# Kernel tuning notes

Hardware: AMD Instinct MI355X
Metric: run time of the kernel (lower is better)

Reference implementation:

```python
import math
import jax, jax.numpy as jnp
import numpy as np

NH = 16          # num attention heads
NOPE = 128       # qk_nope_head_dim
ROPE = 64        # qk_rope_head_dim
VD = 128         # v_head_dim
QLR = 1536       # q_lora_rank
IH = 8           # index_n_heads
ID = 128         # index_head_dim
TOPK = 8         # index_topk
EPS = 1e-5


def layernorm(x, w, b):
    mu = jnp.mean(x, axis=-1, keepdims=True)
    var = jnp.mean((x - mu) ** 2, axis=-1, keepdims=True)
    return (x - mu) * jax.lax.rsqrt(var + EPS) * w + b


def rope_tables(dim, end, base=10000.0):
    freqs = 1.0 / (base ** (jnp.arange(0, dim, 2, dtype=jnp.float32) / dim))  # [dim//2]
    t = jnp.arange(end, dtype=jnp.float32)
    f = jnp.outer(t, freqs)  # [end, dim//2]
    return jnp.cos(f), jnp.sin(f)


def apply_rope(x, cos, sin):
    # x: [b, h, s, d]; cos/sin: [s, d//2] (interleaved real/imag pairs)
    xr, xi = x[..., 0::2], x[..., 1::2]
    c = cos[None, None, :, :]
    s = sin[None, None, :, :]
    or_, oi = xr * c - xi * s, xr * s + xi * c
    return jnp.stack([or_, oi], axis=-1).reshape(x.shape)


def setup_inputs() -> dict:
    key = jax.random.key(0)
    ks = jax.random.split(key, 16)
    H = 2048
    B, S = 2, 2048
    w = lambda k, shp: (jax.random.normal(k, shp, dtype=jnp.float32) * 0.02)
    return {
        "x": jax.random.normal(ks[0], (B, S, H), dtype=jnp.float32),
        "W_cq": w(ks[1], (H, QLR)),
        "q_norm_w": jnp.ones((QLR,), jnp.float32),
        "q_norm_b": jnp.zeros((QLR,), jnp.float32),
        "W_q": w(ks[2], (QLR, NH * (NOPE + ROPE))),
        "W_ckv": w(ks[3], (H, NH * (NOPE + ROPE))),
        "kv_norm_w": jnp.ones((NOPE,), jnp.float32),
        "kv_norm_b": jnp.zeros((NOPE,), jnp.float32),
        "W_kv": w(ks[4], (NOPE, NOPE + VD)),
        "W_o": w(ks[5], (NH * VD, H)),
        "W_ip": w(ks[6], (H, IH * ID)),
        "W_ig": w(ks[7], (H, IH)),
        "W_sq": w(ks[8], (ID, ID)),
        "W_sk": w(ks[9], (ID, ID)),
        "W_sv": w(ks[10], (ID, ID)),
        "W_io": w(ks[11], (ID, H)),
    }


def _forward(x, W_cq, q_norm_w, q_norm_b, W_q, W_ckv, kv_norm_w, kv_norm_b,
             W_kv, W_o, W_ip, W_ig, W_sq, W_sk, W_sv, W_io):
    B, S, H = x.shape
    # --- MLA dense path ---
    qc = layernorm(x @ W_cq, q_norm_w, q_norm_b)                  # [B,S,QLR]
    qp = (qc @ W_q).reshape(B, S, NH, NOPE + ROPE).transpose(0, 2, 1, 3)
    q_nope, q_pe = qp[..., :NOPE], qp[..., NOPE:]
    kvc = (x @ W_ckv).reshape(B, S, NH, ROPE + NOPE).transpose(0, 2, 1, 3)
    k_pe, kv_nope = kvc[..., :ROPE], kvc[..., ROPE:]
    kv_n = layernorm(kv_nope, kv_norm_w, kv_norm_b)               # [B,NH,S,NOPE]
    kvp = kv_n @ W_kv                                             # [B,NH,S,NOPE+VD]
    k_nope, v = kvp[..., :NOPE], kvp[..., NOPE:]
    cos, sin = rope_tables(ROPE, S)
    q_pe = apply_rope(q_pe, cos, sin)
    k_pe = apply_rope(k_pe, cos, sin)
    q = jnp.concatenate([q_nope, q_pe], axis=-1)                  # [B,NH,S,192]
    k = jnp.concatenate([k_nope, k_pe], axis=-1)
    scale = 1.0 / math.sqrt(NOPE + ROPE)
    scores = jnp.einsum("bhqd,bhkd->bhqk", q, k) * scale
    causal = jnp.triu(jnp.ones((S, S), dtype=bool), k=1)
    scores = jnp.where(causal[None, None], -jnp.inf, scores)
    probs = jax.nn.softmax(scores.astype(jnp.float32), axis=-1).astype(q.dtype)
    attn = jnp.einsum("bhqk,bhkd->bhqd", probs, v)                # [B,NH,S,VD]
    # --- NSA sparse path (lightning indexer) ---
    ist = (x @ W_ip).reshape(B, S, IH, ID).transpose(0, 2, 1, 3)  # [B,IH,S,ID]
    gate = (x @ W_ig).transpose(0, 2, 1)                          # [B,IH,S]
    _, top_idx = jax.lax.top_k(gate, TOPK)                        # [B,IH,TOPK]
    sel = jnp.take_along_axis(ist, top_idx[..., None], axis=2)    # [B,IH,TOPK,ID]
    sq, sk, sv = sel @ W_sq, sel @ W_sk, sel @ W_sv
    ss = jnp.einsum("bhqd,bhkd->bhqk", sq, sk) / math.sqrt(ID)    # [B,IH,TOPK,TOPK]
    sp = jax.nn.softmax(ss.astype(jnp.float32), axis=-1).astype(sq.dtype)
    so = jnp.einsum("bhqk,bhkd->bhqd", sp, sv)                    # [B,IH,TOPK,ID]
    sparse_out = so @ W_io                                        # [B,IH,TOPK,H]
    io = sparse_out.mean(axis=2)[:, :, None, :VD]                 # [B,IH,1,VD]
    io = jnp.broadcast_to(io, (B, IH, S, VD))
    io = jnp.repeat(io, NH // IH, axis=1)                         # [B,NH,S,VD]
    attn = attn + io
    out = attn.transpose(0, 2, 1, 3).reshape(B, S, NH * VD) @ W_o
    return out


def reference(x, W_cq, q_norm_w, q_norm_b, W_q, W_ckv, kv_norm_w, kv_norm_b,
              W_kv, W_o, W_ip, W_ig, W_sq, W_sk, W_sv, W_io):
    return _forward(x, W_cq, q_norm_w, q_norm_b, W_q, W_ckv, kv_norm_w,
                    kv_norm_b, W_kv, W_o, W_ip, W_ig, W_sq, W_sk, W_sv, W_io)
```

## Files before the change

kernel.cpp:

```cpp
#include <hip/hip_runtime.h>
#include <hip/hip_bf16.h>
#include <math.h>

#define NH    16
#define NOPE  128
#define ROPED 64
#define VD    128
#define QLR   1536
#define IH    8
#define ID    128
#define TOPK  8
#define EPSF  1e-5f
#define B_    2
#define S_    2048
#define H_    2048

using bf16 = __hip_bfloat16;
typedef __attribute__((ext_vector_type(8))) short short8;
typedef __attribute__((ext_vector_type(4))) short short4v;
typedef __attribute__((ext_vector_type(4))) float f32x4;

#define GLOBAL_AS __attribute__((address_space(1)))
#define LDS_AS    __attribute__((address_space(3)))

__device__ __forceinline__ float b2f(bf16 v) { return __bfloat162float(v); }
__device__ __forceinline__ bf16 f2b(float v) { return __float2bfloat16(v); }
__device__ __forceinline__ void stoC(float* p, float v) { *p = v; }
__device__ __forceinline__ void stoC(bf16* p, float v) { *p = __float2bfloat16(v); }

__global__ __launch_bounds__(256) void gate_k(const float* __restrict__ x,
                                              const float* __restrict__ Wg,
                                              float* __restrict__ gate) {
    const int t = threadIdx.x;
    const int wid = t >> 6, lane = t & 63;
    const int row = blockIdx.x * 4 + wid;
    const float* xp = x + (size_t)row * H_;

    float acc[8] = {};
    for (int k0 = 0; k0 < H_; k0 += 256) {
        const int kb = k0 + lane * 4;
        const f32x4 xv = *(const f32x4*)(xp + kb);
        const f32x4 w0 = *(const f32x4*)(Wg + (size_t)kb * 8);
        const f32x4 w1 = *(const f32x4*)(Wg + (size_t)kb * 8 + 4);
        const f32x4 w2 = *(const f32x4*)(Wg + (size_t)(kb + 1) * 8);
        const f32x4 w3 = *(const f32x4*)(Wg + (size_t)(kb + 1) * 8 + 4);
        const f32x4 w4 = *(const f32x4*)(Wg + (size_t)(kb + 2) * 8);
        const f32x4 w5 = *(const f32x4*)(Wg + (size_t)(kb + 2) * 8 + 4);
        const f32x4 w6 = *(const f32x4*)(Wg + (size_t)(kb + 3) * 8);
        const f32x4 w7 = *(const f32x4*)(Wg + (size_t)(kb + 3) * 8 + 4);
#pragma unroll
        for (int j = 0; j < 4; j++) {
            acc[j]     += xv[0] * w0[j] + xv[1] * w2[j] + xv[2] * w4[j] + xv[3] * w6[j];
            acc[4 + j] += xv[0] * w1[j] + xv[1] * w3[j] + xv[2] * w5[j] + xv[3] * w7[j];
        }
    }
#pragma unroll
    for (int j = 0; j < 8; j++) {
#pragma unroll
        for (int off = 32; off > 0; off >>= 1)
            acc[j] += __shfl_xor(acc[j], off);
    }
    if (lane == 0) {
#pragma unroll
        for (int j = 0; j < 8; j++) gate[(size_t)row * 8 + j] = acc[j];
    }
}

template <typename OT>
__global__ __launch_bounds__(256) void gemm_bt_mfma_k(const bf16* __restrict__ A,
                                                      const bf16* __restrict__ Bt,
                                                      OT* __restrict__ C,
                                                      int M, int N, int K) {
    __shared__ bf16 As[128 * 32];
    __shared__ bf16 Bs[128 * 32];
    const int t = threadIdx.x;
    const int w = t >> 6;
    const int l = t & 63;
    const int col = l & 15;
    const int quad = l >> 4;
    const int wm = w >> 1, wn = w & 1;

    const int gx = gridDim.x;
    const int nwg = gx * gridDim.y;
    const int lin = blockIdx.y * gx + blockIdx.x;
    const int work = (lin & 7) * (nwg >> 3) + (lin >> 3);
    const int row0 = (work / gx) * 128;
    const int col0 = (work % gx) * 128;

    const int rA = l >> 2;
    const int cA = (l & 3) * 8;
    const bf16* ga0 = A + (size_t)(row0 + w * 16 + rA) * K + cA;
    const bf16* ga1 = A + (size_t)(row0 + (4 + w) * 16 + rA) * K + cA;
    const bf16* gb0 = Bt + (size_t)(col0 + w * 16 + rA) * K + cA;
    const bf16* gb1 = Bt + (size_t)(col0 + (4 + w) * 16 + rA) * K + cA;
    bf16* lA0 = &As[w * 512];
    bf16* lA1 = &As[(4 + w) * 512];
    bf16* lB0 = &Bs[w * 512];
    bf16* lB1 = &Bs[(4 + w) * 512];

    f32x4 acc[4][4];
#pragma unroll
    for (int i = 0; i < 4; i++)
#pragma unroll
        for (int j = 0; j < 4; j++) acc[i][j] = (f32x4){0.f, 0.f, 0.f, 0.f};

    for (int k0 = 0; k0 < K; k0 += 32) {
        __syncthreads();
        __builtin_amdgcn_global_load_lds((const GLOBAL_AS void*)(ga0 + k0),
                                         (LDS_AS void*)lA0, 16, 0, 0);
        __builtin_amdgcn_global_load_lds((const GLOBAL_AS void*)(ga1 + k0),
                                         (LDS_AS void*)lA1, 16, 0, 0);
        __builtin_amdgcn_global_load_lds((const GLOBAL_AS void*)(gb0 + k0),
                                         (LDS_AS void*)lB0, 16, 0, 0);
        __builtin_amdgcn_global_load_lds((const GLOBAL_AS void*)(gb1 + k0),
                                         (LDS_AS void*)lB1, 16, 0, 0);
        __syncthreads();

        short8 af[4], bfr[4];
#pragma unroll
        for (int i = 0; i < 4; i++) {
            af[i]  = *(const short8*)&As[(wm * 64 + i * 16 + col) * 32 + quad * 8];
            bfr[i] = *(const short8*)&Bs[(wn * 64 + i * 16 + col) * 32 + quad * 8];
        }
#pragma unroll
        for (int i = 0; i < 4; i++)
#pragma unroll
            for (int j = 0; j < 4; j++)
                acc[i][j] = __builtin_amdgcn_mfma_f32_16x16x32_bf16(af[i], bfr[j], acc[i][j], 0, 0, 0);
    }

#pragma unroll
    for (int i = 0; i < 4; i++)
#pragma unroll
        for (int j = 0; j < 4; j++)
#pragma unroll
            for (int r = 0; r < 4; r++) {
                const int gr = row0 + wm * 64 + i * 16 + quad * 4 + r;
                const int gc = col0 + wn * 64 + j * 16 + col;
                stoC(C + (size_t)gr * N + gc, acc[i][j][r]);
            }
}

__global__ __launch_bounds__(256) void gemm_kv_k(const bf16* __restrict__ A,
                                                 const bf16* __restrict__ Bt,
                                                 bf16* __restrict__ kvc,
                                                 bf16* __restrict__ VbT) {
    __shared__ bf16 As[128 * 32];
    __shared__ bf16 Bs[128 * 32];
    const int K = 128;
    const int t = threadIdx.x;
    const int w = t >> 6;
    const int l = t & 63;
    const int col = l & 15;
    const int quad = l >> 4;
    const int wm = w >> 1, wn = w & 1;

    const int gx = gridDim.x;
    const int nwg = gx * gridDim.y;
    const int lin = blockIdx.y * gx + blockIdx.x;
    const int work = (lin & 7) * (nwg >> 3) + (lin >> 3);
    const int row0 = (work / gx) * 128;
    const int col0 = (work % gx) * 128;

    const int rA = l >> 2;
    const int cA = (l & 3) * 8;
    const bf16* ga0 = A + (size_t)(row0 + w * 16 + rA) * K + cA;
    const bf16* ga1 = A + (size_t)(row0 + (4 + w) * 16 + rA) * K + cA;
    const bf16* gb0 = Bt + (size_t)(col0 + w * 16 + rA) * K + cA;
    const bf16* gb1 = Bt + (size_t)(col0 + (4 + w) * 16 + rA) * K + cA;
    bf16* lA0 = &As[w * 512];
    bf16* lA1 = &As[(4 + w) * 512];
    bf16* lB0 = &Bs[w * 512];
    bf16* lB1 = &Bs[(4 + w) * 512];

    f32x4 acc[4][4];
#pragma unroll
    for (int i = 0; i < 4; i++)
#pragma unroll
        for (int j = 0; j < 4; j++) acc[i][j] = (f32x4){0.f, 0.f, 0.f, 0.f};

    for (int k0 = 0; k0 < K; k0 += 32) {
        __syncthreads();
        __builtin_amdgcn_global_load_lds((const GLOBAL_AS void*)(ga0 + k0),
                                         (LDS_AS void*)lA0, 16, 0, 0);
        __builtin_amdgcn_global_load_lds((const GLOBAL_AS void*)(ga1 + k0),
                                         (LDS_AS void*)lA1, 16, 0, 0);
        __builtin_amdgcn_global_load_lds((const GLOBAL_AS void*)(gb0 + k0),
                                         (LDS_AS void*)lB0, 16, 0, 0);
        __builtin_amdgcn_global_load_lds((const GLOBAL_AS void*)(gb1 + k0),
                                         (LDS_AS void*)lB1, 16, 0, 0);
        __syncthreads();

        short8 af[4], bfr[4];
#pragma unroll
        for (int i = 0; i < 4; i++) {
            af[i]  = *(const short8*)&As[(wm * 64 + i * 16 + col) * 32 + quad * 8];
            bfr[i] = *(const short8*)&Bs[(wn * 64 + i * 16 + col) * 32 + quad * 8];
        }
#pragma unroll
        for (int i = 0; i < 4; i++)
#pragma unroll
            for (int j = 0; j < 4; j++)
                acc[i][j] = __builtin_amdgcn_mfma_f32_16x16x32_bf16(af[i], bfr[j], acc[i][j], 0, 0, 0);
    }

    if (col0 == 0) {
#pragma unroll
        for (int i = 0; i < 4; i++)
#pragma unroll
            for (int j = 0; j < 4; j++)
#pragma unroll
                for (int r = 0; r < 4; r++) {
                    const int gr = row0 + wm * 64 + i * 16 + quad * 4 + r;
                    const int gc = wn * 64 + j * 16 + col;
                    kvc[(size_t)gr * 192 + gc] = f2b(acc[i][j][r]);
                }
    } else {
        const int bb = row0 >> 15;
        const int ssb = ((row0 >> 4) & (S_ - 1)) + wm * 4;
#pragma unroll
        for (int j = 0; j < 4; j++) {
            const int dv = wn * 64 + j * 16 + col;
#pragma unroll
            for (int r = 0; r < 4; r++) {
                const int hh = quad * 4 + r;
                short4v pk;
#pragma unroll
                for (int i = 0; i < 4; i++) {
                    bf16 v = f2b(acc[i][j][r]);
                    pk[i] = *(short*)&v;
                }
                *(short4v*)&VbT[((size_t)(bb * NH + hh) * 128 + dv) * S_ + ssb] = pk;
            }
        }
    }
}

__global__ __launch_bounds__(256) void kv_ln_k(bf16* __restrict__ kvc,
                                               const float* __restrict__ knw,
                                               const float* __restrict__ knb,
                                               bf16* __restrict__ kvn) {
    const int idx = blockIdx.x * 4 + (threadIdx.x >> 6);
    const int lane = threadIdx.x & 63;
    const int s = (idx >> 4) & (S_ - 1);
    const size_t base = (size_t)idx * 192;

    const float v0 = b2f(kvc[base + 64 + lane]);
    const float v1 = b2f(kvc[base + 128 + lane]);
    float xr = 0.f, xi = 0.f;
    if (lane < 32) { xr = b2f(kvc[base + 2 * lane]); xi = b2f(kvc[base + 2 * lane + 1]); }

    float s1 = v0 + v1, s2 = v0 * v0 + v1 * v1;
#pragma unroll
    for (int off = 32; off > 0; off >>= 1) {
        s1 += __shfl_xor(s1, off);
        s2 += __shfl_xor(s2, off);
    }
    const float mu = s1 * (1.f / 128.f);
    const float rinv = rsqrtf(s2 * (1.f / 128.f) - mu * mu + EPSF);
    kvn[(size_t)idx * 128 + lane]      = f2b((v0 - mu) * rinv * knw[lane] + knb[lane]);
    kvn[(size_t)idx * 128 + lane + 64] = f2b((v1 - mu) * rinv * knw[lane + 64] + knb[lane + 64]);

    if (lane < 32) {
        const float freq = exp2f(-0.41524101186092014f * (float)lane);
        const float ang = (float)s * freq;
        float sn, c; sincosf(ang, &sn, &c);
        kvc[base + 128 + 2 * lane]     = f2b(xr * c - xi * sn);
        kvc[base + 128 + 2 * lane + 1] = f2b(xr * sn + xi * c);
    }
}

__global__ __launch_bounds__(256) void cast_bf16_k(const float* __restrict__ X,
                                                   bf16* __restrict__ Y, int n4) {
    for (int i = blockIdx.x * 256 + threadIdx.x; i < n4; i += gridDim.x * 256) {
        const f32x4 v = ((const f32x4*)X)[i];
        short4v o;
#pragma unroll
        for (int j = 0; j < 4; j++) {
            bf16 b = f2b(v[j]);
            o[j] = *(short*)&b;
        }
        ((short4v*)Y)[i] = o;
    }
}

__global__ __launch_bounds__(256) void transpose_cast_k(const float* __restrict__ W,
                                                        bf16* __restrict__ Wt,
                                                        int K, int N) {
    __shared__ float tile[32][33];
    const int t = threadIdx.x;
    const int tx = t & 31, ty = t >> 5;
    const int n0 = blockIdx.x * 32;
    const int k0 = blockIdx.y * 32;
#pragma unroll
    for (int i = 0; i < 4; i++)
        tile[ty + 8 * i][tx] = W[(size_t)(k0 + ty + 8 * i) * N + n0 + tx];
    __syncthreads();
#pragma unroll
    for (int i = 0; i < 4; i++)
        Wt[(size_t)(n0 + ty + 8 * i) * K + k0 + tx] = f2b(tile[tx][ty + 8 * i]);
}

__global__ __launch_bounds__(256) void layernorm_cast_k(const float* __restrict__ X,
                                                        const float* __restrict__ w,
                                                        const float* __restrict__ b,
                                                        bf16* __restrict__ Y,
                                                        int L) {
    __shared__ float r1[256], r2[256];
    const int row = blockIdx.x;
    const int t = threadIdx.x;
    const float* xp = X + (size_t)row * L;
    bf16* yp = Y + (size_t)row * L;
    float s1 = 0.f, s2 = 0.f;
    for (int j = t; j < L; j += 256) { const float v = xp[j]; s1 += v; s2 += v * v; }
    r1[t] = s1; r2[t] = s2; __syncthreads();
    for (int off = 128; off > 0; off >>= 1) {
        if (t < off) { r1[t] += r1[t + off]; r2[t] += r2[t + off]; }
        __syncthreads();
    }
    const float mu   = r1[0] / (float)L;
    const float var  = r2[0] / (float)L - mu * mu;
    const float rinv = rsqrtf(var + EPSF);
    for (int j = t; j < L; j += 256)
        yp[j] = f2b((xp[j] - mu) * rinv * w[j] + b[j]);
}

__global__ __launch_bounds__(256) void q_rope_k(bf16* __restrict__ qp) {
    const int total = B_ * S_ * NH * 32;
    for (int p = blockIdx.x * 256 + threadIdx.x; p < total; p += gridDim.x * 256) {
        const int j = p & 31;
        const int row = p >> 5;
        const int sr = row >> 4;
        const int s = sr & (S_ - 1);
        const size_t base = (size_t)row * 192 + 128 + 2 * j;
        const float xr = b2f(qp[base]);
        const float xi = b2f(qp[base + 1]);
        const float freq = exp2f(-0.41524101186092014f * (float)j);
        const float ang = (float)s * freq;
        float sn, c; sincosf(ang, &sn, &c);
        qp[base]     = f2b(xr * c - xi * sn);
        qp[base + 1] = f2b(xr * sn + xi * c);
    }
}

__global__ __launch_bounds__(256) void sparse_k(const float* __restrict__ gate,
                                                const float* __restrict__ ist,
                                                const float* __restrict__ Wsq,
                                                const float* __restrict__ Wsk,
                                                const float* __restrict__ Wsv,
                                                const float* __restrict__ Wio,
                                                float* __restrict__ io) {
    __shared__ float g[S_];
    __shared__ float sel[TOPK][ID];
    __shared__ float sq[TOPK][ID], sk[TOPK][ID], sv[TOPK][ID];
    __shared__ float sp[TOPK][TOPK];
    __shared__ float ms[ID];
    __shared__ float rv[256];
    __shared__ int ri[256];
    __shared__ int sidx[TOPK];
    const int bi = blockIdx.x;
    const int ih = bi % IH;
    const int b = bi / IH;
    const int t = threadIdx.x;

    for (int s = t; s < S_; s += 256) g[s] = gate[(size_t)(b * S_ + s) * IH + ih];
    __syncthreads();

    for (int r = 0; r < TOPK; r++) {
        float bv = -INFINITY; int bx = S_;
        for (int s = t; s < S_; s += 256) {
            const float v = g[s];
            if (v > bv) { bv = v; bx = s; }
        }
        rv[t] = bv; ri[t] = bx; __syncthreads();
        for (int off = 128; off > 0; off >>= 1) {
            if (t < off) {
                const float v2 = rv[t + off]; const int i2 = ri[t + off];
                if (v2 > rv[t] || (v2 == rv[t] && i2 < ri[t])) { rv[t] = v2; ri[t] = i2; }
            }
            __syncthreads();
        }
        if (t == 0) { sidx[r] = ri[0]; g[ri[0]] = -INFINITY; }
        __syncthreads();
    }

    for (int i = t; i < TOPK * ID; i += 256) {
        const int r = i >> 7, d = i & 127;
        sel[r][d] = ist[((size_t)(b * S_ + sidx[r]) * IH + ih) * ID + d];
    }
    __syncthreads();

    for (int i = t; i < TOPK * ID; i += 256) {
        const int r = i >> 7, n = i & 127;
        float aq = 0.f, ak = 0.f, av = 0.f;
        for (int k = 0; k < 128; k++) {
            const float s = sel[r][k];
            aq += s * Wsq[k * ID + n];
            ak += s * Wsk[k * ID + n];
            av += s * Wsv[k * ID + n];
        }
        sq[r][n] = aq; sk[r][n] = ak; sv[r][n] = av;
    }
    __syncthreads();

    if (t < TOPK * TOPK) {
        const int r = t >> 3, c = t & 7;
        float a = 0.f;
        for (int k = 0; k < 128; k++) a += sq[r][k] * sk[c][k];
        sp[r][c] = a * 0.08838834764831845f;
    }
    __syncthreads();

    if (t < TOPK) {
        float m = -INFINITY;
        for (int c = 0; c < 8; c++) m = fmaxf(m, sp[t][c]);
        float e[8]; float sum = 0.f;
        for (int c = 0; c < 8; c++) { e[c] = expf(sp[t][c] - m); sum += e[c]; }
        for (int c = 0; c < 8; c++) sp[t][c] = e[c] / sum;
    }
    __syncthreads();

    if (t < ID) {
        float acc = 0.f;
        for (int r = 0; r < 8; r++) {
            float so = 0.f;
            for (int c = 0; c < 8; c++) so += sp[r][c] * sv[c][t];
            acc += so;
        }
        ms[t] = acc * 0.125f;
    }
    __syncthreads();

    if (t < ID) {
        float acc = 0.f;
        for (int k = 0; k < 128; k++) acc += ms[k] * Wio[(size_t)k * H_ + t];
        io[((size_t)b * IH + ih) * ID + t] = acc;
    }
}

__global__ __launch_bounds__(256, 2) void attn_mfma_k(const bf16* __restrict__ Qp,
                                                      const bf16* __restrict__ Kc,
                                                      const bf16* __restrict__ VbT,
                                                      const float* __restrict__ io,
                                                      bf16* __restrict__ O) {
    __shared__ unsigned short Kt[64 * 200];
    __shared__ unsigned short Vt[128 * 72];
    __shared__ unsigned short Ps[4 * 16 * 72];

    const int lin = blockIdx.x + 16 * blockIdx.y + 256 * blockIdx.z;
    const int swz = (lin & 7) * 64 + (lin >> 3);
    const int pairi = swz & 15;
    const int h = (swz >> 4) & 15;
    const int b = swz >> 8;

    const int t = threadIdx.x;
    const int lane = t & 63;
    const int wq = t >> 6;
    const int col = lane & 15;
    const int quad = lane >> 4;

    const float scale = 0.07216878364870322f;
    const bf16* vplane = VbT + (size_t)(b * NH + h) * 128 * (size_t)S_;

    const int kr = t >> 2;
    const int kc0 = (t & 3) * 48;
    const int vki0 = (t & 7) * 8;
    const int vdv = t >> 3;

#pragma unroll 1
    for (int ti = 0; ti < 2; ti++) {
        const int qt = (ti == 0) ? pairi : 31 - pairi;
        const int q0 = qt * 64;

        short8 qfrag[6];
        {
            const int q = q0 + wq * 16 + col;
            const short8* qrow = (const short8*)(Qp + ((size_t)(b * S_ + q) * NH + h) * 192);
#pragma unroll
            for (int kc = 0; kc < 6; kc++) qfrag[kc] = qrow[kc * 4 + quad];
        }

        float m_r[4], l_r[4];
#pragma unroll
        for (int r = 0; r < 4; r++) { m_r[r] = -1e30f; l_r[r] = 0.f; }
        f32x4 accO[8];
#pragma unroll
        for (int nt = 0; nt < 8; nt++) accO[nt] = (f32x4){0.f, 0.f, 0.f, 0.f};

        const int nkt = qt + 1;

        short8 kreg[6], vreg[4];
        {
            const short8* ksrc = (const short8*)(Kc + ((size_t)(b * S_ + kr) * NH + h) * 192 + kc0);
#pragma unroll
            for (int c = 0; c < 6; c++) kreg[c] = ksrc[c];
#pragma unroll
            for (int p = 0; p < 4; p++)
                vreg[p] = *(const short8*)(vplane + (size_t)(p * 32 + vdv) * S_ + vki0);
        }

        for (int kt = 0; kt < nkt; kt++) {
            const int kt0 = kt * 64;
            __syncthreads();
            {
                short8* dst = (short8*)&Kt[kr * 200 + kc0];
#pragma unroll
                for (int c = 0; c < 6; c++) dst[c] = kreg[c];
#pragma unroll
                for (int p = 0; p < 4; p++)
                    *(short8*)&Vt[(p * 32 + vdv) * 72 + vki0] = vreg[p];
            }
            __syncthreads();

            if (kt + 1 < nkt) {
                const int nk0 = kt0 + 64;
                const short8* ksrc = (const short8*)(Kc + ((size_t)(b * S_ + nk0 + kr) * NH + h) * 192 + kc0);
#pragma unroll
                for (int c = 0; c < 6; c++) kreg[c] = ksrc[c];
#pragma unroll
                for (int p = 0; p < 4; p++)
                    vreg[p] = *(const short8*)(vplane + (size_t)(p * 32 + vdv) * S_ + nk0 + vki0);
            }

            f32x4 s[4];
            __builtin_amdgcn_s_setprio(1);
#pragma unroll
            for (int nt = 0; nt < 4; nt++) {
                f32x4 acc = (f32x4){0.f, 0.f, 0.f, 0.f};
#pragma unroll
                for (int kc = 0; kc < 6; kc++) {
                    const short8 kf = *(const short8*)&Kt[(nt * 16 + col) * 200 + kc * 32 + quad * 8];
                    acc = __builtin_amdgcn_mfma_f32_16x16x32_bf16(qfrag[kc], kf, acc, 0, 0, 0);
                }
                s[nt] = acc;
            }
            __builtin_amdgcn_s_setprio(0);
#pragma unroll
            for (int nt = 0; nt < 4; nt++)
#pragma unroll
                for (int r = 0; r < 4; r++) {
                    const int kg = kt0 + nt * 16 + col;
                    const int qg = q0 + wq * 16 + quad * 4 + r;
                    const float v = s[nt][r] * scale;
                    s[nt][r] = (kg > qg) ? -1e30f : v;
                }
            float alpha[4];
#pragma unroll
            for (int r = 0; r < 4; r++) {
                float mt = fmaxf(fmaxf(s[0][r], s[1][r]), fmaxf(s[2][r], s[3][r]));
                mt = fmaxf(mt, __shfl_xor(mt, 1));
                mt = fmaxf(mt, __shfl_xor(mt, 2));
                mt = fmaxf(mt, __shfl_xor(mt, 4));
                mt = fmaxf(mt, __shfl_xor(mt, 8));
                const bool need = (mt > m_r[r] + 8.f);
                const float mn = need ? mt : m_r[r];
                alpha[r] = need ? __expf(m_r[r] - mn) : 1.f;
                m_r[r] = mn;
                float rs = 0.f;
#pragma unroll
                for (int nt = 0; nt < 4; nt++) {
                    const float p = __expf(s[nt][r] - mn);
                    s[nt][r] = p;
                    rs += p;
                }
                rs += __shfl_xor(rs, 1);
                rs += __shfl_xor(rs, 2);
                rs += __shfl_xor(rs, 4);
                rs += __shfl_xor(rs, 8);
                l_r[r] = l_r[r] * alpha[r] + rs;
            }
            {
                unsigned short* pw = &Ps[wq * 1152];
#pragma unroll
                for (int nt = 0; nt < 4; nt++)
#pragma unroll
                    for (int r = 0; r < 4; r++) {
                        bf16 hv = f2b(s[nt][r]);
                        pw[(quad * 4 + r) * 72 + nt * 16 + col] = *(unsigned short*)&hv;
                    }
            }
            short8 pf[2];
#pragma unroll
            for (int kk = 0; kk < 2; kk++)
                pf[kk] = *(const short8*)&Ps[wq * 1152 + col * 72 + kk * 32 + quad * 8];
            if (!(alpha[0] == 1.f && alpha[1] == 1.f && alpha[2] == 1.f && alpha[3] == 1.f)) {
#pragma unroll
                for (int nt = 0; nt < 8; nt++)
#pragma unroll
                    for (int r = 0; r < 4; r++) accO[nt][r] *= alpha[r];
            }
            __builtin_amdgcn_s_setprio(1);
#pragma unroll
            for (int nt = 0; nt < 8; nt++) {
#pragma unroll
                for (int kk = 0; kk < 2; kk++) {
                    const short8 vf = *(const short8*)&Vt[(nt * 16 + col) * 72 + kk * 32 + quad * 8];
                    accO[nt] = __builtin_amdgcn_mfma_f32_16x16x32_bf16(pf[kk], vf, accO[nt], 0, 0, 0);
                }
            }
            __builtin_amdgcn_s_setprio(0);
        }

        const float* iorow = io + ((size_t)b * IH + (h >> 1)) * ID;
        float rinv[4];
#pragma unroll
        for (int r = 0; r < 4; r++) rinv[r] = 1.f / l_r[r];
#pragma unroll
        for (int nt = 0; nt < 8; nt++) {
            const int dv = nt * 16 + col;
            const float iov = iorow[dv];
#pragma unroll
            for (int r = 0; r < 4; r++) {
                const int q = q0 + wq * 16 + quad * 4 + r;
                O[((size_t)(b * S_ + q) * NH + h) * VD + dv] = f2b(accO[nt][r] * rinv[r] + iov);
            }
        }
    }
}

extern "C" void kernel_launch(void* const* d_in, const int* in_sizes, int n_in,
                              void* d_out, int out_size, void* d_ws, size_t ws_size,
                              hipStream_t stream) {
    const float* x      = (const float*)d_in[0];
    const float* W_cq   = (const float*)d_in[1];
    const float* qn_w   = (const float*)d_in[2];
    const float* qn_b   = (const float*)d_in[3];
    const float* W_q    = (const float*)d_in[4];
    const float* W_ckv  = (const float*)d_in[5];
    const float* kvn_w  = (const float*)d_in[6];
    const float* kvn_b  = (const float*)d_in[7];
    const float* W_kv   = (const float*)d_in[8];
    const float* W_o    = (const float*)d_in[9];
    const float* W_ip   = (const float*)d_in[10];
    const float* W_ig   = (const float*)d_in[11];
    const float* W_sq   = (const float*)d_in[12];
    const float* W_sk   = (const float*)d_in[13];
    const float* W_sv   = (const float*)d_in[14];
    const float* W_io   = (const float*)d_in[15];
    float* out = (float*)d_out;

    const int M = B_ * S_;

    char* wsb = (char*)d_ws;
    float* rbig  = (float*)wsb;
    bf16*  kvn   = (bf16*)(wsb + 16777216);
    bf16*  qp    = (bf16*)(wsb + 33554432);
    bf16*  kvc   = (bf16*)(wsb + 58720256);
    bf16*  cqb   = (bf16*)(wsb + 58720256);
    bf16*  VbT   = (bf16*)(wsb + 83886080);
    bf16*  Wt    = (bf16*)(wsb + 83886080);
    float* gate  = (float*)(wsb + 100663296);
    bf16*  WkvT  = (bf16*)(wsb + 100663296);
    float* iob   = (float*)(wsb + 100794368);
    float* cq    = rbig;
    float* ist   = rbig;
    bf16*  attnb = (bf16*)rbig;
    bf16*  xb    = (bf16*)d_out;

    dim3 blk(256);

    cast_bf16_k<<<dim3(2048), blk, 0, stream>>>(x, xb, M * H_ / 4);

    transpose_cast_k<<<dim3(QLR / 32, H_ / 32), blk, 0, stream>>>(W_cq, Wt, H_, QLR);
    gemm_bt_mfma_k<float><<<dim3(QLR / 128, M / 128), blk, 0, stream>>>(xb, Wt, cq, M, QLR, H_);
    layernorm_cast_k<<<dim3(M), blk, 0, stream>>>(cq, qn_w, qn_b, cqb, QLR);

    transpose_cast_k<<<dim3(3072 / 32, QLR / 32), blk, 0, stream>>>(W_q, Wt, QLR, 3072);
    gemm_bt_mfma_k<bf16><<<dim3(3072 / 128, M / 128), blk, 0, stream>>>(cqb, Wt, qp, M, 3072, QLR);

    transpose_cast_k<<<dim3(3072 / 32, H_ / 32), blk, 0, stream>>>(W_ckv, Wt, H_, 3072);
    gemm_bt_mfma_k<bf16><<<dim3(3072 / 128, M / 128), blk, 0, stream>>>(xb, Wt, kvc, M, 3072, H_);

    transpose_cast_k<<<dim3(1024 / 32, H_ / 32), blk, 0, stream>>>(W_ip, Wt, H_, 1024);
    gemm_bt_mfma_k<float><<<dim3(1024 / 128, M / 128), blk, 0, stream>>>(xb, Wt, ist, M, IH * ID, H_);

    gate_k<<<dim3(M / 4), blk, 0, stream>>>(x, W_ig, gate);

    q_rope_k<<<dim3(2048), blk, 0, stream>>>(qp);

    kv_ln_k<<<dim3(B_ * S_ * NH / 4), blk, 0, stream>>>(kvc, kvn_w, kvn_b, kvn);

    sparse_k<<<dim3(B_ * IH), blk, 0, stream>>>(gate, ist, W_sq, W_sk, W_sv, W_io, iob);

    transpose_cast_k<<<dim3(256 / 32, 128 / 32), blk, 0, stream>>>(W_kv, WkvT, 128, 256);
    gemm_kv_k<<<dim3(2, (B_ * S_ * NH) / 128), blk, 0, stream>>>(kvn, WkvT, kvc, VbT);

    attn_mfma_k<<<dim3(16, NH, B_), blk, 0, stream>>>(qp, kvc, VbT, iob, attnb);

    transpose_cast_k<<<dim3(H_ / 32, H_ / 32), blk, 0, stream>>>(W_o, Wt, H_, H_);
    gemm_bt_mfma_k<float><<<dim3(H_ / 128, M / 128), blk, 0, stream>>>(attnb, Wt, out, M, H_, H_);
}
```

Before: 691.8 us.

## Fuse the three x-projection GEMMs and launch attention per query tile

Concatenates the transposed W_cq, W_ckv and W_ip weights into one matrix so a single GEMM over x computes cq, kvc and ist, with the epilogue routing each column range to its own buffer. The attention kernel no longer pairs two query tiles per block; it launches 1024 blocks, one per query tile, ordered longest causal tile first. The workspace layout is reorganised so the combined transposed weights, W_q and W_o transposes can live alongside the intermediates. This cuts launch count, raises GEMM occupancy and improves load balance, at the cost of more workspace aliasing and less per-block reuse in attention.

```diff
diff --git a/kernel.cpp b/kernel.cpp
--- a/kernel.cpp
+++ b/kernel.cpp
@@ -138,6 +138,85 @@
                 const int gr = row0 + wm * 64 + i * 16 + quad * 4 + r;
                 const int gc = col0 + wn * 64 + j * 16 + col;
                 stoC(C + (size_t)gr * N + gc, acc[i][j][r]);
+            }
+}
+
+__global__ __launch_bounds__(256) void gemm_x3_k(const bf16* __restrict__ A,
+                                                 const bf16* __restrict__ Bt,
+                                                 float* __restrict__ cq,
+                                                 bf16* __restrict__ kvc,
+                                                 float* __restrict__ ist) {
+    __shared__ bf16 As[128 * 32];
+    __shared__ bf16 Bs[128 * 32];
+    const int K = H_;
+    const int t = threadIdx.x;
+    const int w = t >> 6;
+    const int l = t & 63;
+    const int col = l & 15;
+    const int quad = l >> 4;
+    const int wm = w >> 1, wn = w & 1;
+
+    const int gx = gridDim.x;
+    const int nwg = gx * gridDim.y;
+    const int lin = blockIdx.y * gx + blockIdx.x;
+    const int work = (lin & 7) * (nwg >> 3) + (lin >> 3);
+    const int row0 = (work / gx) * 128;
+    const int col0 = (work % gx) * 128;
+
+    const int rA = l >> 2;
+    const int cA = (l & 3) * 8;
+    const bf16* ga0 = A + (size_t)(row0 + w * 16 + rA) * K + cA;
+    const bf16* ga1 = A + (size_t)(row0 + (4 + w) * 16 + rA) * K + cA;
+    const bf16* gb0 = Bt + (size_t)(col0 + w * 16 + rA) * K + cA;
+    const bf16* gb1 = Bt + (size_t)(col0 + (4 + w) * 16 + rA) * K + cA;
+    bf16* lA0 = &As[w * 512];
+    bf16* lA1 = &As[(4 + w) * 512];
+    bf16* lB0 = &Bs[w * 512];
+    bf16* lB1 = &Bs[(4 + w) * 512];
+
+    f32x4 acc[4][4];
+#pragma unroll
+    for (int i = 0; i < 4; i++)
+#pragma unroll
+        for (int j = 0; j < 4; j++) acc[i][j] = (f32x4){0.f, 0.f, 0.f, 0.f};
+
+    for (int k0 = 0; k0 < K; k0 += 32) {
+        __syncthreads();
+        __builtin_amdgcn_global_load_lds((const GLOBAL_AS void*)(ga0 + k0),
+                                         (LDS_AS void*)lA0, 16, 0, 0);
+        __builtin_amdgcn_global_load_lds((const GLOBAL_AS void*)(ga1 + k0),
+                                         (LDS_AS void*)lA1, 16, 0, 0);
+        __builtin_amdgcn_global_load_lds((const GLOBAL_AS void*)(gb0 + k0),
+                                         (LDS_AS void*)lB0, 16, 0, 0);
+        __builtin_amdgcn_global_load_lds((const GLOBAL_AS void*)(gb1 + k0),
+                                         (LDS_AS void*)lB1, 16, 0, 0);
+        __syncthreads();
+
+        short8 af[4], bfr[4];
+#pragma unroll
+        for (int i = 0; i < 4; i++) {
+            af[i]  = *(const short8*)&As[(wm * 64 + i * 16 + col) * 32 + quad * 8];
+            bfr[i] = *(const short8*)&Bs[(wn * 64 + i * 16 + col) * 32 + quad * 8];
+        }
+#pragma unroll
+        for (int i = 0; i < 4; i++)
+#pragma unroll
+            for (int j = 0; j < 4; j++)
+                acc[i][j] = __builtin_amdgcn_mfma_f32_16x16x32_bf16(af[i], bfr[j], acc[i][j], 0, 0, 0);
+    }
+
+#pragma unroll
+    for (int i = 0; i < 4; i++)
+#pragma unroll
+        for (int j = 0; j < 4; j++)
+#pragma unroll
+            for (int r = 0; r < 4; r++) {
+                const int gr = row0 + wm * 64 + i * 16 + quad * 4 + r;
+                const int gc = col0 + wn * 64 + j * 16 + col;
+                const float v = acc[i][j][r];
+                if (col0 < 1536)       cq[(size_t)gr * QLR + gc] = v;
+                else if (col0 < 4608)  kvc[(size_t)gr * 3072 + (gc - 1536)] = f2b(v);
+                else                   ist[(size_t)gr * 1024 + (gc - 4608)] = v;
             }
 }
 
@@ -447,11 +526,12 @@
     __shared__ unsigned short Vt[128 * 72];
     __shared__ unsigned short Ps[4 * 16 * 72];
 
-    const int lin = blockIdx.x + 16 * blockIdx.y + 256 * blockIdx.z;
-    const int swz = (lin & 7) * 64 + (lin >> 3);
-    const int pairi = swz & 15;
-    const int h = (swz >> 4) & 15;
-    const int b = swz >> 8;
+    const int lin = blockIdx.x;
+    const int qt = 31 - (lin >> 5);
+    const int hb = lin & 31;
+    const int h = hb & 15;
+    const int b = hb >> 4;
+    const int q0 = qt * 64;
 
     const int t = threadIdx.x;
     const int lane = t & 63;
@@ -467,153 +547,147 @@
     const int vki0 = (t & 7) * 8;
     const int vdv = t >> 3;
 
-#pragma unroll 1
-    for (int ti = 0; ti < 2; ti++) {
-        const int qt = (ti == 0) ? pairi : 31 - pairi;
-        const int q0 = qt * 64;
-
-        short8 qfrag[6];
+    short8 qfrag[6];
+    {
+        const int q = q0 + wq * 16 + col;
+        const short8* qrow = (const short8*)(Qp + ((size_t)(b * S_ + q) * NH + h) * 192);
+#pragma unroll
+        for (int kc = 0; kc < 6; kc++) qfrag[kc] = qrow[kc * 4 + quad];
+    }
+
+    float m_r[4], l_r[4];
+#pragma unroll
+    for (int r = 0; r < 4; r++) { m_r[r] = -1e30f; l_r[r] = 0.f; }
+    f32x4 accO[8];
+#pragma unroll
+    for (int nt = 0; nt < 8; nt++) accO[nt] = (f32x4){0.f, 0.f, 0.f, 0.f};
+
+    const int nkt = qt + 1;
+
+    short8 kreg[6], vreg[4];
+    {
+        const short8* ksrc = (const short8*)(Kc + ((size_t)(b * S_ + kr) * NH + h) * 192 + kc0);
+#pragma unroll
+        for (int c = 0; c < 6; c++) kreg[c] = ksrc[c];
+#pragma unroll
+        for (int p = 0; p < 4; p++)
+            vreg[p] = *(const short8*)(vplane + (size_t)(p * 32 + vdv) * S_ + vki0);
+    }
+
+    for (int kt = 0; kt < nkt; kt++) {
+        const int kt0 = kt * 64;
+        __syncthreads();
         {
-            const int q = q0 + wq * 16 + col;
-            const short8* qrow = (const short8*)(Qp + ((size_t)(b * S_ + q) * NH + h) * 192);
-#pragma unroll
-            for (int kc = 0; kc < 6; kc++) qfrag[kc] = qrow[kc * 4 + quad];
-        }
-
-        float m_r[4], l_r[4];
-#pragma unroll
-        for (int r = 0; r < 4; r++) { m_r[r] = -1e30f; l_r[r] = 0.f; }
-        f32x4 accO[8];
-#pragma unroll
-        for (int nt = 0; nt < 8; nt++) accO[nt] = (f32x4){0.f, 0.f, 0.f, 0.f};
-
-        const int nkt = qt + 1;
-
-        short8 kreg[6], vreg[4];
+            short8* dst = (short8*)&Kt[kr * 200 + kc0];
+#pragma unroll
+            for (int c = 0; c < 6; c++) dst[c] = kreg[c];
+#pragma unroll
+            for (int p = 0; p < 4; p++)
+                *(short8*)&Vt[(p * 32 + vdv) * 72 + vki0] = vreg[p];
+        }
+        __syncthreads();
+
+        if (kt + 1 < nkt) {
+            const int nk0 = kt0 + 64;
+            const short8* ksrc = (const short8*)(Kc + ((size_t)(b * S_ + nk0 + kr) * NH + h) * 192 + kc0);
+#pragma unroll
+            for (int c = 0; c < 6; c++) kreg[c] = ksrc[c];
+#pragma unroll
+            for (int p = 0; p < 4; p++)
+                vreg[p] = *(const short8*)(vplane + (size_t)(p * 32 + vdv) * S_ + nk0 + vki0);
+        }
+
+        f32x4 s[4];
+        __builtin_amdgcn_s_setprio(1);
+#pragma unroll
+        for (int nt = 0; nt < 4; nt++) {
+            f32x4 acc = (f32x4){0.f, 0.f, 0.f, 0.f};
+#pragma unroll
+            for (int kc = 0; kc < 6; kc++) {
+                const short8 kf = *(const short8*)&Kt[(nt * 16 + col) * 200 + kc * 32 + quad * 8];
+                acc = __builtin_amdgcn_mfma_f32_16x16x32_bf16(qfrag[kc], kf, acc, 0, 0, 0);
+            }
+            s[nt] = acc;
+        }
+        __builtin_amdgcn_s_setprio(0);
+#pragma unroll
+        for (int nt = 0; nt < 4; nt++)
+#pragma unroll
+            for (int r = 0; r < 4; r++) {
+                const int kg = kt0 + nt * 16 + col;
+                const int qg = q0 + wq * 16 + quad * 4 + r;
+                const float v = s[nt][r] * scale;
+                s[nt][r] = (kg > qg) ? -1e30f : v;
+            }
+        float alpha[4];
+#pragma unroll
+        for (int r = 0; r < 4; r++) {
+            float mt = fmaxf(fmaxf(s[0][r], s[1][r]), fmaxf(s[2][r], s[3][r]));
+            mt = fmaxf(mt, __shfl_xor(mt, 1));
+            mt = fmaxf(mt, __shfl_xor(mt, 2));
+            mt = fmaxf(mt, __shfl_xor(mt, 4));
+            mt = fmaxf(mt, __shfl_xor(mt, 8));
+            const bool need = (mt > m_r[r] + 8.f);
+            const float mn = need ? mt : m_r[r];
+            alpha[r] = need ? __expf(m_r[r] - mn) : 1.f;
+            m_r[r] = mn;
+            float rs = 0.f;
+#pragma unroll
+            for (int nt = 0; nt < 4; nt++) {
+                const float p = __expf(s[nt][r] - mn);
+                s[nt][r] = p;
+                rs += p;
+            }
+            rs += __shfl_xor(rs, 1);
+            rs += __shfl_xor(rs, 2);
+            rs += __shfl_xor(rs, 4);
+            rs += __shfl_xor(rs, 8);
+            l_r[r] = l_r[r] * alpha[r] + rs;
+        }
         {
-            const short8* ksrc = (const short8*)(Kc + ((size_t)(b * S_ + kr) * NH + h) * 192 + kc0);
-#pragma unroll
-            for (int c = 0; c < 6; c++) kreg[c] = ksrc[c];
-#pragma unroll
-            for (int p = 0; p < 4; p++)
-                vreg[p] = *(const short8*)(vplane + (size_t)(p * 32 + vdv) * S_ + vki0);
-        }
-
-        for (int kt = 0; kt < nkt; kt++) {
-            const int kt0 = kt * 64;
-            __syncthreads();
-            {
-                short8* dst = (short8*)&Kt[kr * 200 + kc0];
-#pragma unroll
-                for (int c = 0; c < 6; c++) dst[c] = kreg[c];
-#pragma unroll
-                for (int p = 0; p < 4; p++)
-                    *(short8*)&Vt[(p * 32 + vdv) * 72 + vki0] = vreg[p];
+            unsigned short* pw = &Ps[wq * 1152];
+#pragma unroll
+            for (int nt = 0; nt < 4; nt++)
+#pragma unroll
+                for (int r = 0; r < 4; r++) {
+                    bf16 hv = f2b(s[nt][r]);
+                    pw[(quad * 4 + r) * 72 + nt * 16 + col] = *(unsigned short*)&hv;
+                }
+        }
+        short8 pf[2];
+#pragma unroll
+        for (int kk = 0; kk < 2; kk++)
+            pf[kk] = *(const short8*)&Ps[wq * 1152 + col * 72 + kk * 32 + quad * 8];
+        if (!(alpha[0] == 1.f && alpha[1] == 1.f && alpha[2] == 1.f && alpha[3] == 1.f)) {
+#pragma unroll
+            for (int nt = 0; nt < 8; nt++)
+#pragma unroll
+                for (int r = 0; r < 4; r++) accO[nt][r] *= alpha[r];
+        }
+        __builtin_amdgcn_s_setprio(1);
+#pragma unroll
+        for (int nt = 0; nt < 8; nt++) {
+#pragma unroll
+            for (int kk = 0; kk < 2; kk++) {
+                const short8 vf = *(const short8*)&Vt[(nt * 16 + col) * 72 + kk * 32 + quad * 8];
+                accO[nt] = __builtin_amdgcn_mfma_f32_16x16x32_bf16(pf[kk], vf, accO[nt], 0, 0, 0);
             }
-            __syncthreads();
-
-            if (kt + 1 < nkt) {
-                const int nk0 = kt0 + 64;
-                const short8* ksrc = (const short8*)(Kc + ((size_t)(b * S_ + nk0 + kr) * NH + h) * 192 + kc0);
-#pragma unroll
-                for (int c = 0; c < 6; c++) kreg[c] = ksrc[c];
-#pragma unroll
-                for (int p = 0; p < 4; p++)
-                    vreg[p] = *(const short8*)(vplane + (size_t)(p * 32 + vdv) * S_ + nk0 + vki0);
-            }
-
-            f32x4 s[4];
-            __builtin_amdgcn_s_setprio(1);
-#pragma unroll
-            for (int nt = 0; nt < 4; nt++) {
-                f32x4 acc = (f32x4){0.f, 0.f, 0.f, 0.f};
-#pragma unroll
-                for (int kc = 0; kc < 6; kc++) {
-                    const short8 kf = *(const short8*)&Kt[(nt * 16 + col) * 200 + kc * 32 + quad * 8];
-                    acc = __builtin_amdgcn_mfma_f32_16x16x32_bf16(qfrag[kc], kf, acc, 0, 0, 0);
-                }
-                s[nt] = acc;
-            }
-            __builtin_amdgcn_s_setprio(0);
-#pragma unroll
-            for (int nt = 0; nt < 4; nt++)
-#pragma unroll
-                for (int r = 0; r < 4; r++) {
-                    const int kg = kt0 + nt * 16 + col;
-                    const int qg = q0 + wq * 16 + quad * 4 + r;
-                    const float v = s[nt][r] * scale;
-                    s[nt][r] = (kg > qg) ? -1e30f : v;
-                }
-            float alpha[4];
-#pragma unroll
-            for (int r = 0; r < 4; r++) {
-                float mt = fmaxf(fmaxf(s[0][r], s[1][r]), fmaxf(s[2][r], s[3][r]));
-                mt = fmaxf(mt, __shfl_xor(mt, 1));
-                mt = fmaxf(mt, __shfl_xor(mt, 2));
-                mt = fmaxf(mt, __shfl_xor(mt, 4));
-                mt = fmaxf(mt, __shfl_xor(mt, 8));
-                const bool need = (mt > m_r[r] + 8.f);
-                const float mn = need ? mt : m_r[r];
-                alpha[r] = need ? __expf(m_r[r] - mn) : 1.f;
-                m_r[r] = mn;
-                float rs = 0.f;
-#pragma unroll
-                for (int nt = 0; nt < 4; nt++) {
-                    const float p = __expf(s[nt][r] - mn);
-                    s[nt][r] = p;
-                    rs += p;
-                }
-                rs += __shfl_xor(rs, 1);
-                rs += __shfl_xor(rs, 2);
-                rs += __shfl_xor(rs, 4);
-                rs += __shfl_xor(rs, 8);
-                l_r[r] = l_r[r] * alpha[r] + rs;
-            }
-            {
-                unsigned short* pw = &Ps[wq * 1152];
-#pragma unroll
-                for (int nt = 0; nt < 4; nt++)
-#pragma unroll
-                    for (int r = 0; r < 4; r++) {
-                        bf16 hv = f2b(s[nt][r]);
-                        pw[(quad * 4 + r) * 72 + nt * 16 + col] = *(unsigned short*)&hv;
-                    }
-            }
-            short8 pf[2];
-#pragma unroll
-            for (int kk = 0; kk < 2; kk++)
-                pf[kk] = *(const short8*)&Ps[wq * 1152 + col * 72 + kk * 32 + quad * 8];
-            if (!(alpha[0] == 1.f && alpha[1] == 1.f && alpha[2] == 1.f && alpha[3] == 1.f)) {
-#pragma unroll
-                for (int nt = 0; nt < 8; nt++)
-#pragma unroll
-                    for (int r = 0; r < 4; r++) accO[nt][r] *= alpha[r];
-            }
-            __builtin_amdgcn_s_setprio(1);
-#pragma unroll
-            for (int nt = 0; nt < 8; nt++) {
-#pragma unroll
-                for (int kk = 0; kk < 2; kk++) {
-                    const short8 vf = *(const short8*)&Vt[(nt * 16 + col) * 72 + kk * 32 + quad * 8];
-                    accO[nt] = __builtin_amdgcn_mfma_f32_16x16x32_bf16(pf[kk], vf, accO[nt], 0, 0, 0);
-                }
-            }
-            __builtin_amdgcn_s_setprio(0);
-        }
-
-        const float* iorow = io + ((size_t)b * IH + (h >> 1)) * ID;
-        float rinv[4];
-#pragma unroll
-        for (int r = 0; r < 4; r++) rinv[r] = 1.f / l_r[r];
-#pragma unroll
-        for (int nt = 0; nt < 8; nt++) {
-            const int dv = nt * 16 + col;
-            const float iov = iorow[dv];
-#pragma unroll
-            for (int r = 0; r < 4; r++) {
-                const int q = q0 + wq * 16 + quad * 4 + r;
-                O[((size_t)(b * S_ + q) * NH + h) * VD + dv] = f2b(accO[nt][r] * rinv[r] + iov);
-            }
+        }
+        __builtin_amdgcn_s_setprio(0);
+    }
+
+    const float* iorow = io + ((size_t)b * IH + (h >> 1)) * ID;
+    float rinv[4];
+#pragma unroll
+    for (int r = 0; r < 4; r++) rinv[r] = 1.f / l_r[r];
+#pragma unroll
+    for (int nt = 0; nt < 8; nt++) {
+        const int dv = nt * 16 + col;
+        const float iov = iorow[dv];
+#pragma unroll
+        for (int r = 0; r < 4; r++) {
+            const int q = q0 + wq * 16 + quad * 4 + r;
+            O[((size_t)(b * S_ + q) * NH + h) * VD + dv] = f2b(accO[nt][r] * rinv[r] + iov);
         }
     }
 }
@@ -642,37 +716,36 @@
     const int M = B_ * S_;
 
     char* wsb = (char*)d_ws;
-    float* rbig  = (float*)wsb;
-    bf16*  kvn   = (bf16*)(wsb + 16777216);
+    bf16*  WtM   = (bf16*)wsb;
+    bf16*  cqb   = (bf16*)wsb;
+    bf16*  WqT   = (bf16*)(wsb + 12582912);
+    bf16*  kvn   = (bf16*)wsb;
+    bf16*  attnb = (bf16*)wsb;
+    bf16*  WoT   = (bf16*)(wsb + 16777216);
+    float* cq    = (float*)(wsb + 33554432);
     bf16*  qp    = (bf16*)(wsb + 33554432);
     bf16*  kvc   = (bf16*)(wsb + 58720256);
-    bf16*  cqb   = (bf16*)(wsb + 58720256);
+    float* ist   = (float*)(wsb + 83886080);
     bf16*  VbT   = (bf16*)(wsb + 83886080);
-    bf16*  Wt    = (bf16*)(wsb + 83886080);
     float* gate  = (float*)(wsb + 100663296);
     bf16*  WkvT  = (bf16*)(wsb + 100663296);
     float* iob   = (float*)(wsb + 100794368);
-    float* cq    = rbig;
-    float* ist   = rbig;
-    bf16*  attnb = (bf16*)rbig;
     bf16*  xb    = (bf16*)d_out;
 
     dim3 blk(256);
 
     cast_bf16_k<<<dim3(2048), blk, 0, stream>>>(x, xb, M * H_ / 4);
 
-    transpose_cast_k<<<dim3(QLR / 32, H_ / 32), blk, 0, stream>>>(W_cq, Wt, H_, QLR);
-    gemm_bt_mfma_k<float><<<dim3(QLR / 128, M / 128), blk, 0, stream>>>(xb, Wt, cq, M, QLR, H_);
+    transpose_cast_k<<<dim3(QLR / 32, H_ / 32), blk, 0, stream>>>(W_cq, WtM, H_, QLR);
+    transpose_cast_k<<<dim3(3072 / 32, H_ / 32), blk, 0, stream>>>(W_ckv, WtM + (size_t)1536 * H_, H_, 3072);
+    transpose_cast_k<<<dim3(1024 / 32, H_ / 32), blk, 0, stream>>>(W_ip, WtM + (size_t)4608 * H_, H_, 1024);
+
+    gemm_x3_k<<<dim3(5632 / 128, M / 128), blk, 0, stream>>>(xb, WtM, cq, kvc, ist);
+
     layernorm_cast_k<<<dim3(M), blk, 0, stream>>>(cq, qn_w, qn_b, cqb, QLR);
 
-    transpose_cast_k<<<dim3(3072 / 32, QLR / 32), blk, 0, stream>>>(W_q, Wt, QLR, 3072);
-    gemm_bt_mfma_k<bf16><<<dim3(3072 / 128, M / 128), blk, 0, stream>>>(cqb, Wt, qp, M, 3072, QLR);
-
-    transpose_cast_k<<<dim3(3072 / 32, H_ / 32), blk, 0, stream>>>(W_ckv, Wt, H_, 3072);
-    gemm_bt_mfma_k<bf16><<<dim3(3072 / 128, M / 128), blk, 0, stream>>>(xb, Wt, kvc, M, 3072, H_);
-
-    transpose_cast_k<<<dim3(1024 / 32, H_ / 32), blk, 0, stream>>>(W_ip, Wt, H_, 1024);
-    gemm_bt_mfma_k<float><<<dim3(1024 / 128, M / 128), blk, 0, stream>>>(xb, Wt, ist, M, IH * ID, H_);
+    transpose_cast_k<<<dim3(3072 / 32, QLR / 32), blk, 0, stream>>>(W_q, WqT, QLR, 3072);
+    gemm_bt_mfma_k<bf16><<<dim3(3072 / 128, M / 128), blk, 0, stream>>>(cqb, WqT, qp, M, 3072, QLR);
 
     gate_k<<<dim3(M / 4), blk, 0, stream>>>(x, W_ig, gate);
 
@@ -685,8 +758,8 @@
     transpose_cast_k<<<dim3(256 / 32, 128 / 32), blk, 0, stream>>>(W_kv, WkvT, 128, 256);
     gemm_kv_k<<<dim3(2, (B_ * S_ * NH) / 128), blk, 0, stream>>>(kvn, WkvT, kvc, VbT);
 
-    attn_mfma_k<<<dim3(16, NH, B_), blk, 0, stream>>>(qp, kvc, VbT, iob, attnb);
-
-    transpose_cast_k<<<dim3(H_ / 32, H_ / 32), blk, 0, stream>>>(W_o, Wt, H_, H_);
-    gemm_bt_mfma_k<float><<<dim3(H_ / 128, M / 128), blk, 0, stream>>>(attnb, Wt, out, M, H_, H_);
-}
+    attn_mfma_k<<<dim3(1024), blk, 0, stream>>>(qp, kvc, VbT, iob, attnb);
+
+    transpose_cast_k<<<dim3(H_ / 32, H_ / 32), blk, 0, stream>>>(W_o, WoT, H_, H_);
+    gemm_bt_mfma_k<float><<<dim3(H_ / 128, M / 128), blk, 0, stream>>>(attnb, WoT, out, M, H_, H_);
+}
```

After: 678.9 us. About the same (-1.9%).
